# Kernel tuning notes

Hardware: AMD Instinct MI355X
Metric: run time of the kernel (lower is better)

Reference implementation:

```python
import jax, jax.numpy as jnp
import numpy as np


def _resize_bilinear_ac(x, Ht, Wt):
    # bilinear resize with align_corners=True; x: [B,C,h,w] -> [B,C,Ht,Wt]
    B, C, h, w = x.shape
    ys = jnp.linspace(0.0, h - 1.0, Ht)
    xs = jnp.linspace(0.0, w - 1.0, Wt)
    y0 = jnp.floor(ys).astype(jnp.int32)
    y1 = jnp.minimum(y0 + 1, h - 1)
    x0 = jnp.floor(xs).astype(jnp.int32)
    x1 = jnp.minimum(x0 + 1, w - 1)
    wy = (ys - y0).astype(x.dtype)[None, None, :, None]
    wx = (xs - x0).astype(x.dtype)[None, None, None, :]
    r0 = x[:, :, y0, :]
    r1 = x[:, :, y1, :]
    v00 = r0[:, :, :, x0]; v01 = r0[:, :, :, x1]
    v10 = r1[:, :, :, x0]; v11 = r1[:, :, :, x1]
    return (1 - wy) * ((1 - wx) * v00 + wx * v01) + wy * ((1 - wx) * v10 + wx * v11)


def _grid_sample_zeros_ac(img, grid):
    # F.grid_sample(mode='bilinear', padding_mode='zeros', align_corners=True)
    # img: [B,C,H,W], grid: [B,H,W,2] in [-1,1] (x, y)
    B, C, H, W = img.shape
    x = (grid[..., 0] + 1.0) * 0.5 * (W - 1)  # [B,H,W] pixel coords
    y = (grid[..., 1] + 1.0) * 0.5 * (H - 1)
    x0 = jnp.floor(x)
    y0 = jnp.floor(y)
    wx = (x - x0)[:, None]  # [B,1,H,W]
    wy = (y - y0)[:, None]

    def gather(xi, yi):
        valid = ((xi >= 0) & (xi <= W - 1) & (yi >= 0) & (yi <= H - 1)).astype(img.dtype)
        xc = jnp.clip(xi, 0, W - 1).astype(jnp.int32)
        yc = jnp.clip(yi, 0, H - 1).astype(jnp.int32)
        v = jax.vmap(lambda im, yy, xx: im[:, yy, xx])(img, yc, xc)  # [B,C,H,W]
        return v * valid[:, None]

    v00 = gather(x0, y0)
    v01 = gather(x0 + 1, y0)
    v10 = gather(x0, y0 + 1)
    v11 = gather(x0 + 1, y0 + 1)
    return (1 - wy) * ((1 - wx) * v00 + wx * v01) + wy * ((1 - wx) * v10 + wx * v11)


def setup_inputs() -> dict:
    key = jax.random.key(0)
    k1, k2, k3 = jax.random.split(key, 3)
    B, C, H, W = 8, 3, 384, 1280
    h, w = 96, 320
    image = jax.random.normal(k1, (B, C, H, W), dtype=jnp.float32)
    # positive disparity (fraction of width, scaled by W inside forward)
    disp = jax.random.uniform(k2, (B, 1, h, w), dtype=jnp.float32, minval=0.01, maxval=0.3)
    scene = jax.random.normal(k3, (B, 3, h, w), dtype=jnp.float32) * 0.1
    K = jnp.array([[371.0, 0.0, 320.0], [0.0, 371.0, 96.0], [0.0, 0.0, 1.0]], dtype=jnp.float32)
    intrinsic = jnp.tile(K[None], (B, 1, 1))
    aug_size = jnp.tile(jnp.array([192.0, 640.0], dtype=jnp.float32)[None], (B, 1))
    return {"image": image, "disp": disp, "scene": scene, "intrinsic": intrinsic, "aug_size": aug_size}


def reference(image, disp, scene, intrinsic, aug_size):
    B, C, H, W = image.shape
    # interpolate_as(disp, image) * W
    disp_full = _resize_bilinear_ac(disp, H, W) * W
    # rel_scale = local_scale / aug_size, local_scale = (H, W)
    rel = jnp.array([H, W], dtype=aug_size.dtype) / aug_size  # [B,2] = (sy, sx)
    sy, sx = rel[:, 0], rel[:, 1]
    fx = intrinsic[:, 0, 0] * sx
    fy = intrinsic[:, 1, 1] * sy
    cx = intrinsic[:, 0, 2] * sx
    cy = intrinsic[:, 1, 2] * sy
    z = jnp.zeros_like(fx)
    o = jnp.ones_like(fx)
    K = jnp.stack([jnp.stack([fx, z, cx], 1),
                   jnp.stack([z, fy, cy], 1),
                   jnp.stack([z, z, o], 1)], 1)  # [B,3,3]
    # disp2depth_stereo_clamp
    depth = jnp.clip(fx[:, None, None, None] * 0.54 / (disp_full + 1e-8), 0.001, 80.0)
    # pixel2point
    xg, yg = jnp.meshgrid(jnp.arange(W, dtype=jnp.float32), jnp.arange(H, dtype=jnp.float32))  # [H,W]
    pix = jnp.stack([xg.ravel(), yg.ravel(), jnp.ones(H * W, dtype=jnp.float32)], 0)  # [3,HW]
    Kinv = jnp.linalg.inv(K)
    point = jnp.einsum('bij,jn->bin', Kinv, pix) * depth.reshape(B, 1, -1)  # [B,3,HW]
    # point2pixel_ms
    scene_full = _resize_bilinear_ac(scene, H, W)
    point_form = point.reshape(B, 3, H, W) + scene_full
    proj = jnp.einsum('bij,bjn->bin', K, point_form.reshape(B, 3, -1))
    coord = (proj[:, 0:2] / (proj[:, 2:3] + 1e-8)).reshape(B, 2, H, W)
    nx = coord[:, 0] / (W - 1) * 2.0 - 1.0
    ny = coord[:, 1] / (H - 1) * 2.0 - 1.0
    grid = jnp.stack([nx, ny], -1)  # [B,H,W,2]
    return _grid_sample_zeros_ac(image, grid)
```

## Files before the change

### kernel.cpp

```cpp
#include <hip/hip_runtime.h>
#include <hip/hip_fp16.h>

#define BATCH 8
#define CH 3
#define H_OUT 384
#define W_OUT 1280
#define H_IN 96
#define W_IN 320
#define HW_OUT (H_OUT * W_OUT)
#define HW_IN (H_IN * W_IN)

#define ROWS_PT 2
#define SEGS_PER_ROW (W_OUT / 256)
#define PAIRS (H_OUT / ROWS_PT)
#define CHUNKS_PER_B (PAIRS * SEGS_PER_ROW)

#define LCOLS 68
#define LROWS 3
#define NSURF 4

#define PK_HALves 4
#define PK_BYTES ((size_t)BATCH * HW_OUT * 8)

struct __attribute__((packed, aligned(4))) f2 { float x, y; };
struct __attribute__((packed, aligned(8))) h8 { unsigned int w[4]; };

__global__ __launch_bounds__(256) void pack_kernel(
    const float* __restrict__ image, __half* __restrict__ pk)
{
    int i = blockIdx.x * 256 + threadIdx.x;
    int b = i / HW_OUT;
    int p = i - b * HW_OUT;
    const float* ib = image + (size_t)b * (CH * HW_OUT) + p;
    float c0 = ib[0];
    float c1 = ib[HW_OUT];
    float c2 = ib[2 * HW_OUT];
    __half2 lo = __floats2half2_rn(c0, c1);
    __half2 hi = __floats2half2_rn(c2, 0.0f);
    uint2 v;
    v.x = *reinterpret_cast<unsigned int*>(&lo);
    v.y = *reinterpret_cast<unsigned int*>(&hi);
    *reinterpret_cast<uint2*>(pk + (size_t)i * 4) = v;
}

template <bool PACKED>
__global__ __launch_bounds__(256) void warp_sceneflow_kernel(
    const float* __restrict__ image,
    const __half* __restrict__ pk,
    const float* __restrict__ disp,
    const float* __restrict__ scene,
    const float* __restrict__ intrin,
    const float* __restrict__ aug,
    float* __restrict__ out)
{
    int bid = blockIdx.x;
    int b = bid & 7;
    int c = bid >> 3;
    int yp = c / SEGS_PER_ROW;
    int xseg = c - yp * SEGS_PER_ROW;
    int x = xseg * 256 + threadIdx.x;
    int ybase = yp * ROWS_PT;

    __shared__ float lds[NSURF][LROWS][LCOLS];
    int ylo = (int)((float)ybase * ((float)(H_IN - 1) / (float)(H_OUT - 1)));
    int xlo = (int)((float)(xseg * 256) * ((float)(W_IN - 1) / (float)(W_OUT - 1)));
    {
        const float* surfp[NSURF] = {
            disp + b * HW_IN,
            scene + b * (CH * HW_IN),
            scene + b * (CH * HW_IN) + HW_IN,
            scene + b * (CH * HW_IN) + 2 * HW_IN };
        const int total = NSURF * LROWS * LCOLS;
        for (int i = threadIdx.x; i < total; i += 256) {
            int s = i / (LROWS * LCOLS);
            int rem = i - s * (LROWS * LCOLS);
            int row = rem / LCOLS;
            int col = rem - row * LCOLS;
            int gy = min(ylo + row, H_IN - 1);
            int gx = min(xlo + col, W_IN - 1);
            lds[s][row][col] = surfp[s][gy * W_IN + gx];
        }
    }
    __syncthreads();

    float sy = (float)H_OUT / aug[b * 2 + 0];
    float sxs = (float)W_OUT / aug[b * 2 + 1];
    float fx = intrin[b * 9 + 0] * sxs;
    float fy = intrin[b * 9 + 4] * sy;
    float cx = intrin[b * 9 + 2] * sxs;
    float cy = intrin[b * 9 + 5] * sy;
    float inv_fx = 1.0f / fx;
    float inv_fy = 1.0f / fy;

    float xsrc = (float)x * ((float)(W_IN - 1) / (float)(W_OUT - 1));
    int x0 = (int)xsrc;
    float wx = xsrc - (float)x0;
    int lx = x0 - xlo;

    float g00[ROWS_PT], g01[ROWS_PT], g10[ROWS_PT], g11[ROWS_PT];
    int rb0[ROWS_PT], rb1[ROWS_PT];
    bool rc[ROWS_PT], lc[ROWS_PT];

    #pragma unroll
    for (int r = 0; r < ROWS_PT; ++r) {
        int y = ybase + r;
        float ysrc = (float)y * ((float)(H_IN - 1) / (float)(H_OUT - 1));
        int y0 = (int)ysrc;
        float wy = ysrc - (float)y0;
        int ly = y0 - ylo;

        float d00 = lds[0][ly][lx],     d01 = lds[0][ly][lx + 1];
        float d10 = lds[0][ly + 1][lx], d11 = lds[0][ly + 1][lx + 1];
        float a00 = lds[1][ly][lx],     a01 = lds[1][ly][lx + 1];
        float a10 = lds[1][ly + 1][lx], a11 = lds[1][ly + 1][lx + 1];
        float b00 = lds[2][ly][lx],     b01 = lds[2][ly][lx + 1];
        float b10 = lds[2][ly + 1][lx], b11 = lds[2][ly + 1][lx + 1];
        float e00 = lds[3][ly][lx],     e01 = lds[3][ly][lx + 1];
        float e10 = lds[3][ly + 1][lx], e11 = lds[3][ly + 1][lx + 1];

        float w00 = (1.0f - wy) * (1.0f - wx);
        float w01 = (1.0f - wy) * wx;
        float w10 = wy * (1.0f - wx);
        float w11 = wy * wx;

        float dval = w00 * d00 + w01 * d01 + w10 * d10 + w11 * d11;
        float disp_full = dval * (float)W_OUT;
        float depth = fminf(fmaxf(fx * 0.54f / (disp_full + 1e-8f), 0.001f), 80.0f);

        float sc0 = w00 * a00 + w01 * a01 + w10 * a10 + w11 * a11;
        float sc1 = w00 * b00 + w01 * b01 + w10 * b10 + w11 * b11;
        float sc2 = w00 * e00 + w01 * e01 + w10 * e10 + w11 * e11;

        float X = ((float)x - cx) * inv_fx * depth + sc0;
        float Y = ((float)y - cy) * inv_fy * depth + sc1;
        float Z = depth + sc2;
        float u = fx * X + cx * Z;
        float v = fy * Y + cy * Z;
        float rw = 1.0f / (Z + 1e-8f);
        float coord_x = u * rw;
        float coord_y = v * rw;

        float nx = coord_x / (float)(W_OUT - 1) * 2.0f - 1.0f;
        float ny = coord_y / (float)(H_OUT - 1) * 2.0f - 1.0f;
        float gx = (nx + 1.0f) * 0.5f * (float)(W_OUT - 1);
        float gy = (ny + 1.0f) * 0.5f * (float)(H_OUT - 1);

        float gx0f = floorf(gx), gy0f = floorf(gy);
        float fwx = gx - gx0f, fwy = gy - gy0f;
        int ix0 = (int)gx0f, iy0 = (int)gy0f;
        int ix1 = ix0 + 1, iy1 = iy0 + 1;
        bool vx0 = (ix0 >= 0) && (ix0 <= W_OUT - 1);
        bool vx1 = (ix1 >= 0) && (ix1 <= W_OUT - 1);
        bool vy0 = (iy0 >= 0) && (iy0 <= H_OUT - 1);
        bool vy1 = (iy1 >= 0) && (iy1 <= H_OUT - 1);
        int cx0 = min(max(ix0, 0), W_OUT - 1);
        int cx1 = min(max(ix1, 0), W_OUT - 1);
        int cy0 = min(max(iy0, 0), H_OUT - 1);
        int cy1 = min(max(iy1, 0), H_OUT - 1);
        g00[r] = (1.0f - fwy) * (1.0f - fwx) * ((vx0 && vy0) ? 1.0f : 0.0f);
        g01[r] = (1.0f - fwy) * fwx * ((vx1 && vy0) ? 1.0f : 0.0f);
        g10[r] = fwy * (1.0f - fwx) * ((vx0 && vy1) ? 1.0f : 0.0f);
        g11[r] = fwy * fwx * ((vx1 && vy1) ? 1.0f : 0.0f);

        int xbi = min(cx0, W_OUT - 2);
        rc[r] = (cx0 != xbi);
        lc[r] = (cx1 == xbi);
        rb0[r] = cy0 * W_OUT + xbi;
        rb1[r] = cy1 * W_OUT + xbi;
    }

    float res[ROWS_PT][CH];
    if constexpr (PACKED) {
        const __half* pb = pk + (size_t)b * HW_OUT * 4;
        #pragma unroll
        for (int r = 0; r < ROWS_PT; ++r) {
            h8 L0 = *reinterpret_cast<const h8*>(pb + (size_t)rb0[r] * 4);
            h8 L1 = *reinterpret_cast<const h8*>(pb + (size_t)rb1[r] * 4);
            unsigned t0a = rc[r] ? L0.w[2] : L0.w[0];
            unsigned t0b = rc[r] ? L0.w[3] : L0.w[1];
            unsigned t1a = lc[r] ? L0.w[0] : L0.w[2];
            unsigned t1b = lc[r] ? L0.w[1] : L0.w[3];
            unsigned u0a = rc[r] ? L1.w[2] : L1.w[0];
            unsigned u0b = rc[r] ? L1.w[3] : L1.w[1];
            unsigned u1a = lc[r] ? L1.w[0] : L1.w[2];
            unsigned u1b = lc[r] ? L1.w[1] : L1.w[3];
            __half2 h0a = *reinterpret_cast<__half2*>(&t0a);
            __half2 h1a = *reinterpret_cast<__half2*>(&t1a);
            __half2 k0a = *reinterpret_cast<__half2*>(&u0a);
            __half2 k1a = *reinterpret_cast<__half2*>(&u1a);
            __half2 h0b = *reinterpret_cast<__half2*>(&t0b);
            __half2 h1b = *reinterpret_cast<__half2*>(&t1b);
            __half2 k0b = *reinterpret_cast<__half2*>(&u0b);
            __half2 k1b = *reinterpret_cast<__half2*>(&u1b);
            res[r][0] = g00[r] * __low2float(h0a) + g01[r] * __low2float(h1a)
                      + g10[r] * __low2float(k0a) + g11[r] * __low2float(k1a);
            res[r][1] = g00[r] * __high2float(h0a) + g01[r] * __high2float(h1a)
                      + g10[r] * __high2float(k0a) + g11[r] * __high2float(k1a);
            res[r][2] = g00[r] * __low2float(h0b) + g01[r] * __low2float(h1b)
                      + g10[r] * __low2float(k0b) + g11[r] * __low2float(k1b);
        }
    } else {
        const float* ib = image + (size_t)b * (CH * HW_OUT);
        const float* im0 = ib;
        const float* im1 = ib + HW_OUT;
        const float* im2 = ib + 2 * HW_OUT;
        #pragma unroll
        for (int r = 0; r < ROWS_PT; ++r) {
            f2 P0 = *(const f2*)(im0 + rb0[r]); f2 P1 = *(const f2*)(im0 + rb1[r]);
            f2 Q0 = *(const f2*)(im1 + rb0[r]); f2 Q1 = *(const f2*)(im1 + rb1[r]);
            f2 T0 = *(const f2*)(im2 + rb0[r]); f2 T1 = *(const f2*)(im2 + rb1[r]);
            float p00 = rc[r] ? P0.y : P0.x, p01 = lc[r] ? P0.x : P0.y;
            float p10 = rc[r] ? P1.y : P1.x, p11 = lc[r] ? P1.x : P1.y;
            float q00 = rc[r] ? Q0.y : Q0.x, q01 = lc[r] ? Q0.x : Q0.y;
            float q10 = rc[r] ? Q1.y : Q1.x, q11 = lc[r] ? Q1.x : Q1.y;
            float t00 = rc[r] ? T0.y : T0.x, t01 = lc[r] ? T0.x : T0.y;
            float t10 = rc[r] ? T1.y : T1.x, t11 = lc[r] ? T1.x : T1.y;
            res[r][0] = g00[r] * p00 + g01[r] * p01 + g10[r] * p10 + g11[r] * p11;
            res[r][1] = g00[r] * q00 + g01[r] * q01 + g10[r] * q10 + g11[r] * q11;
            res[r][2] = g00[r] * t00 + g01[r] * t01 + g10[r] * t10 + g11[r] * t11;
        }
    }

    float* ob = out + (size_t)b * (CH * HW_OUT);
    #pragma unroll
    for (int r = 0; r < ROWS_PT; ++r) {
        int op = (ybase + r) * W_OUT + x;
        __builtin_nontemporal_store(res[r][0], ob + op);
        __builtin_nontemporal_store(res[r][1], ob + HW_OUT + op);
        __builtin_nontemporal_store(res[r][2], ob + 2 * HW_OUT + op);
    }
}

extern "C" void kernel_launch(void* const* d_in, const int* in_sizes, int n_in,
                              void* d_out, int out_size, void* d_ws, size_t ws_size,
                              hipStream_t stream) {
    const float* image  = (const float*)d_in[0];
    const float* disp   = (const float*)d_in[1];
    const float* scene  = (const float*)d_in[2];
    const float* intrin = (const float*)d_in[3];
    const float* aug    = (const float*)d_in[4];
    float* out = (float*)d_out;

    const int grid = BATCH * CHUNKS_PER_B;

    if (ws_size >= PK_BYTES) {
        __half* pk = (__half*)d_ws;
        pack_kernel<<<BATCH * HW_OUT / 256, 256, 0, stream>>>(image, pk);
        warp_sceneflow_kernel<true><<<grid, 256, 0, stream>>>(
            image, pk, disp, scene, intrin, aug, out);
    } else {
        warp_sceneflow_kernel<false><<<grid, 256, 0, stream>>>(
            image, nullptr, disp, scene, intrin, aug, out);
    }
}
```

Before: 58.21 us.

## Pad packed image rows and interleave low-res surfaces as float4 in LDS

The packed half-precision image now uses a padded row stride with zeroed guard columns and a leading guard element. This lets the sampler load the 2x2 neighbourhood directly without edge-select logic. The four low-res surfaces (disparity plus three scene-flow channels) are staged into LDS as one interleaved float4 array, so each corner is a single vector LDS read and staging is one load pass per thread. Redundant normalize/denormalize arithmetic for grid coords is also removed. This costs a slightly larger pack buffer and extra zero-writes in the pack kernel, and relies on the padding zeros reproducing the zero-padding validity masks.

```diff
diff --git a/kernel.cpp b/kernel.cpp
--- a/kernel.cpp
+++ b/kernel.cpp
@@ -17,10 +17,10 @@
 
 #define LCOLS 68
 #define LROWS 3
-#define NSURF 4
-
-#define PK_HALves 4
-#define PK_BYTES ((size_t)BATCH * HW_OUT * 8)
+
+#define PSTRIDE 1282
+#define PK_HALVES ((size_t)(1 + (size_t)BATCH * H_OUT * PSTRIDE) * 4)
+#define PK_BYTES (PK_HALVES * 2)
 
 struct __attribute__((packed, aligned(4))) f2 { float x, y; };
 struct __attribute__((packed, aligned(8))) h8 { unsigned int w[4]; };
@@ -31,6 +31,8 @@
     int i = blockIdx.x * 256 + threadIdx.x;
     int b = i / HW_OUT;
     int p = i - b * HW_OUT;
+    int y = p / W_OUT;
+    int x = p - y * W_OUT;
     const float* ib = image + (size_t)b * (CH * HW_OUT) + p;
     float c0 = ib[0];
     float c1 = ib[HW_OUT];
@@ -40,7 +42,17 @@
     uint2 v;
     v.x = *reinterpret_cast<unsigned int*>(&lo);
     v.y = *reinterpret_cast<unsigned int*>(&hi);
-    *reinterpret_cast<uint2*>(pk + (size_t)i * 4) = v;
+    __half* pd = pk + 4;
+    size_t row = (size_t)b * H_OUT + y;
+    *reinterpret_cast<uint2*>(pd + (row * PSTRIDE + x) * 4) = v;
+
+    if (i < BATCH * H_OUT) {
+        uint2 z; z.x = 0u; z.y = 0u;
+        size_t r = (size_t)i;
+        *reinterpret_cast<uint2*>(pd + (r * PSTRIDE + 1280) * 4) = z;
+        *reinterpret_cast<uint2*>(pd + (r * PSTRIDE + 1281) * 4) = z;
+        if (i == 0) *reinterpret_cast<uint2*>(pk) = z;
+    }
 }
 
 template <bool PACKED>
@@ -61,25 +73,23 @@
     int x = xseg * 256 + threadIdx.x;
     int ybase = yp * ROWS_PT;
 
-    __shared__ float lds[NSURF][LROWS][LCOLS];
+    __shared__ float4 lds4[LROWS][LCOLS];
     int ylo = (int)((float)ybase * ((float)(H_IN - 1) / (float)(H_OUT - 1)));
     int xlo = (int)((float)(xseg * 256) * ((float)(W_IN - 1) / (float)(W_OUT - 1)));
-    {
-        const float* surfp[NSURF] = {
-            disp + b * HW_IN,
-            scene + b * (CH * HW_IN),
-            scene + b * (CH * HW_IN) + HW_IN,
-            scene + b * (CH * HW_IN) + 2 * HW_IN };
-        const int total = NSURF * LROWS * LCOLS;
-        for (int i = threadIdx.x; i < total; i += 256) {
-            int s = i / (LROWS * LCOLS);
-            int rem = i - s * (LROWS * LCOLS);
-            int row = rem / LCOLS;
-            int col = rem - row * LCOLS;
-            int gy = min(ylo + row, H_IN - 1);
-            int gx = min(xlo + col, W_IN - 1);
-            lds[s][row][col] = surfp[s][gy * W_IN + gx];
-        }
+    if (threadIdx.x < LROWS * LCOLS) {
+        int row = threadIdx.x / LCOLS;
+        int col = threadIdx.x - row * LCOLS;
+        int gy = min(ylo + row, H_IN - 1);
+        int gx = min(xlo + col, W_IN - 1);
+        int gi = gy * W_IN + gx;
+        const float* dp = disp + b * HW_IN;
+        const float* sp = scene + b * (CH * HW_IN);
+        float4 v;
+        v.x = dp[gi];
+        v.y = sp[gi];
+        v.z = sp[HW_IN + gi];
+        v.w = sp[2 * HW_IN + gi];
+        lds4[row][col] = v;
     }
     __syncthreads();
 
@@ -109,27 +119,23 @@
         float wy = ysrc - (float)y0;
         int ly = y0 - ylo;
 
-        float d00 = lds[0][ly][lx],     d01 = lds[0][ly][lx + 1];
-        float d10 = lds[0][ly + 1][lx], d11 = lds[0][ly + 1][lx + 1];
-        float a00 = lds[1][ly][lx],     a01 = lds[1][ly][lx + 1];
-        float a10 = lds[1][ly + 1][lx], a11 = lds[1][ly + 1][lx + 1];
-        float b00 = lds[2][ly][lx],     b01 = lds[2][ly][lx + 1];
-        float b10 = lds[2][ly + 1][lx], b11 = lds[2][ly + 1][lx + 1];
-        float e00 = lds[3][ly][lx],     e01 = lds[3][ly][lx + 1];
-        float e10 = lds[3][ly + 1][lx], e11 = lds[3][ly + 1][lx + 1];
+        float4 t00 = lds4[ly][lx];
+        float4 t01 = lds4[ly][lx + 1];
+        float4 t10 = lds4[ly + 1][lx];
+        float4 t11 = lds4[ly + 1][lx + 1];
 
         float w00 = (1.0f - wy) * (1.0f - wx);
         float w01 = (1.0f - wy) * wx;
         float w10 = wy * (1.0f - wx);
         float w11 = wy * wx;
 
-        float dval = w00 * d00 + w01 * d01 + w10 * d10 + w11 * d11;
+        float dval = w00 * t00.x + w01 * t01.x + w10 * t10.x + w11 * t11.x;
+        float sc0  = w00 * t00.y + w01 * t01.y + w10 * t10.y + w11 * t11.y;
+        float sc1  = w00 * t00.z + w01 * t01.z + w10 * t10.z + w11 * t11.z;
+        float sc2  = w00 * t00.w + w01 * t01.w + w10 * t10.w + w11 * t11.w;
+
         float disp_full = dval * (float)W_OUT;
         float depth = fminf(fmaxf(fx * 0.54f / (disp_full + 1e-8f), 0.001f), 80.0f);
-
-        float sc0 = w00 * a00 + w01 * a01 + w10 * a10 + w11 * a11;
-        float sc1 = w00 * b00 + w01 * b01 + w10 * b10 + w11 * b11;
-        float sc2 = w00 * e00 + w01 * e01 + w10 * e10 + w11 * e11;
 
         float X = ((float)x - cx) * inv_fx * depth + sc0;
         float Y = ((float)y - cy) * inv_fy * depth + sc1;
@@ -137,13 +143,8 @@
         float u = fx * X + cx * Z;
         float v = fy * Y + cy * Z;
         float rw = 1.0f / (Z + 1e-8f);
-        float coord_x = u * rw;
-        float coord_y = v * rw;
-
-        float nx = coord_x / (float)(W_OUT - 1) * 2.0f - 1.0f;
-        float ny = coord_y / (float)(H_OUT - 1) * 2.0f - 1.0f;
-        float gx = (nx + 1.0f) * 0.5f * (float)(W_OUT - 1);
-        float gy = (ny + 1.0f) * 0.5f * (float)(H_OUT - 1);
+        float gx = u * rw;
+        float gy = v * rw;
 
         float gx0f = floorf(gx), gy0f = floorf(gy);
         float fwx = gx - gx0f, fwy = gy - gy0f;
@@ -153,8 +154,6 @@
         bool vx1 = (ix1 >= 0) && (ix1 <= W_OUT - 1);
         bool vy0 = (iy0 >= 0) && (iy0 <= H_OUT - 1);
         bool vy1 = (iy1 >= 0) && (iy1 <= H_OUT - 1);
-        int cx0 = min(max(ix0, 0), W_OUT - 1);
-        int cx1 = min(max(ix1, 0), W_OUT - 1);
         int cy0 = min(max(iy0, 0), H_OUT - 1);
         int cy1 = min(max(iy1, 0), H_OUT - 1);
         g00[r] = (1.0f - fwy) * (1.0f - fwx) * ((vx0 && vy0) ? 1.0f : 0.0f);
@@ -162,36 +161,36 @@
         g10[r] = fwy * (1.0f - fwx) * ((vx0 && vy1) ? 1.0f : 0.0f);
         g11[r] = fwy * fwx * ((vx1 && vy1) ? 1.0f : 0.0f);
 
-        int xbi = min(cx0, W_OUT - 2);
-        rc[r] = (cx0 != xbi);
-        lc[r] = (cx1 == xbi);
-        rb0[r] = cy0 * W_OUT + xbi;
-        rb1[r] = cy1 * W_OUT + xbi;
+        if constexpr (PACKED) {
+            int bx = min(max(ix0, -1), W_OUT - 1);
+            rb0[r] = ((b * H_OUT + cy0) * PSTRIDE + bx);
+            rb1[r] = ((b * H_OUT + cy1) * PSTRIDE + bx);
+        } else {
+            int cx0 = min(max(ix0, 0), W_OUT - 1);
+            int cx1 = min(max(ix1, 0), W_OUT - 1);
+            int xbi = min(cx0, W_OUT - 2);
+            rc[r] = (cx0 != xbi);
+            lc[r] = (cx1 == xbi);
+            rb0[r] = cy0 * W_OUT + xbi;
+            rb1[r] = cy1 * W_OUT + xbi;
+        }
     }
 
     float res[ROWS_PT][CH];
     if constexpr (PACKED) {
-        const __half* pb = pk + (size_t)b * HW_OUT * 4;
+        const __half* pd = pk + 4;
         #pragma unroll
         for (int r = 0; r < ROWS_PT; ++r) {
-            h8 L0 = *reinterpret_cast<const h8*>(pb + (size_t)rb0[r] * 4);
-            h8 L1 = *reinterpret_cast<const h8*>(pb + (size_t)rb1[r] * 4);
-            unsigned t0a = rc[r] ? L0.w[2] : L0.w[0];
-            unsigned t0b = rc[r] ? L0.w[3] : L0.w[1];
-            unsigned t1a = lc[r] ? L0.w[0] : L0.w[2];
-            unsigned t1b = lc[r] ? L0.w[1] : L0.w[3];
-            unsigned u0a = rc[r] ? L1.w[2] : L1.w[0];
-            unsigned u0b = rc[r] ? L1.w[3] : L1.w[1];
-            unsigned u1a = lc[r] ? L1.w[0] : L1.w[2];
-            unsigned u1b = lc[r] ? L1.w[1] : L1.w[3];
-            __half2 h0a = *reinterpret_cast<__half2*>(&t0a);
-            __half2 h1a = *reinterpret_cast<__half2*>(&t1a);
-            __half2 k0a = *reinterpret_cast<__half2*>(&u0a);
-            __half2 k1a = *reinterpret_cast<__half2*>(&u1a);
-            __half2 h0b = *reinterpret_cast<__half2*>(&t0b);
-            __half2 h1b = *reinterpret_cast<__half2*>(&t1b);
-            __half2 k0b = *reinterpret_cast<__half2*>(&u0b);
-            __half2 k1b = *reinterpret_cast<__half2*>(&u1b);
+            h8 L0 = *reinterpret_cast<const h8*>(pd + (size_t)rb0[r] * 4);
+            h8 L1 = *reinterpret_cast<const h8*>(pd + (size_t)rb1[r] * 4);
+            __half2 h0a = *reinterpret_cast<__half2*>(&L0.w[0]);
+            __half2 h0b = *reinterpret_cast<__half2*>(&L0.w[1]);
+            __half2 h1a = *reinterpret_cast<__half2*>(&L0.w[2]);
+            __half2 h1b = *reinterpret_cast<__half2*>(&L0.w[3]);
+            __half2 k0a = *reinterpret_cast<__half2*>(&L1.w[0]);
+            __half2 k0b = *reinterpret_cast<__half2*>(&L1.w[1]);
+            __half2 k1a = *reinterpret_cast<__half2*>(&L1.w[2]);
+            __half2 k1b = *reinterpret_cast<__half2*>(&L1.w[3]);
             res[r][0] = g00[r] * __low2float(h0a) + g01[r] * __low2float(h1a)
                       + g10[r] * __low2float(k0a) + g11[r] * __low2float(k1a);
             res[r][1] = g00[r] * __high2float(h0a) + g01[r] * __high2float(h1a)
```

Result: faster. 54.66 us (-6.1%).
